# Performance work log

Hardware: AMD Instinct MI355X
Metric: run time of the kernel (lower is better)

Reference implementation:

```python
import jax, jax.numpy as jnp
import numpy as np

D_MODEL = 2048
N_HEADS = 16
HEAD_DIM = D_MODEL // N_HEADS
ROPE_BASE = 10000.0


def rope(x):
    # x: [b, h, s, d]; matches the torch module exactly:
    # x1 = even dims, x2 = odd dims; output = concat([x1*cos - x2*sin, x1*sin + x2*cos], -1)
    b, h, s, d = x.shape
    theta = 1.0 / ROPE_BASE ** (jnp.arange(0, d, 2, dtype=jnp.float32) / d)  # [d/2]
    angles = jnp.arange(s, dtype=jnp.float32)[:, None] * theta[None, :]       # [s, d/2]
    cos = jnp.cos(angles)[None, None]  # [1,1,s,d/2]
    sin = jnp.sin(angles)[None, None]
    x1, x2 = x[..., ::2], x[..., 1::2]
    return jnp.concatenate([x1 * cos - x2 * sin, x1 * sin + x2 * cos], axis=-1)


def setup_inputs() -> dict:
    key = jax.random.key(0)
    ks = jax.random.split(key, 5)
    b, s = 2, 2048
    x = jax.random.normal(ks[0], (b, s, D_MODEL), dtype=jnp.float32)
    scale_in = 1.0 / np.sqrt(D_MODEL)
    Wqkv = jax.random.normal(ks[1], (D_MODEL, 3 * D_MODEL), dtype=jnp.float32) * scale_in
    bqkv = jnp.zeros((3 * D_MODEL,), dtype=jnp.float32)
    Wo = jax.random.normal(ks[2], (D_MODEL, D_MODEL), dtype=jnp.float32) * scale_in
    bo = jnp.zeros((D_MODEL,), dtype=jnp.float32)
    return {"x": x, "Wqkv": Wqkv, "bqkv": bqkv, "Wo": Wo, "bo": bo}


def reference(x, Wqkv, bqkv, Wo, bo):
    b, s, d = x.shape
    qkv = x @ Wqkv + bqkv                      # [b, s, 3d]
    q, k, v = jnp.split(qkv, 3, axis=-1)
    def to_heads(t):
        return t.reshape(b, s, N_HEADS, HEAD_DIM).transpose(0, 2, 1, 3)  # [b,h,s,hd]
    q, k, v = to_heads(q), to_heads(k), to_heads(v)
    q = rope(q)
    k = rope(k)
    scores = jnp.einsum('bhqd,bhkd->bhqk', q, k) / jnp.sqrt(jnp.float32(HEAD_DIM))
    attn = jax.nn.softmax(scores, axis=-1)
    out = jnp.einsum('bhqk,bhkd->bhqd', attn, v)
    out = out.transpose(0, 2, 1, 3).reshape(b, s, d)
    return out @ Wo + bo
```

## Files before the change

kernel.cpp:

```cpp
#include <hip/hip_runtime.h>
#include <hip/hip_bf16.h>
#include <cstdint>
#include <type_traits>

#define D_MODEL 2048
#define NH 16
#define HD 128
#define SEQ 2048
#define QKV_LD (3 * D_MODEL)

typedef __attribute__((ext_vector_type(8))) short short8;
typedef __attribute__((ext_vector_type(4))) float f32x4;
typedef __attribute__((ext_vector_type(16))) float f32x16;

__device__ __forceinline__ ushort f2bf(float f) {
    union { float f; uint32_t u; } c; c.f = f;
    uint32_t u = c.u;
    uint32_t r = (u + 0x7FFFu + ((u >> 16) & 1u)) >> 16;
    return (ushort)r;
}
__device__ __forceinline__ float bf2f(ushort b) {
    union { uint32_t u; float f; } c; c.u = ((uint32_t)b) << 16;
    return c.f;
}

__global__ void cvt_bf16_kernel(const float* __restrict__ in, ushort* __restrict__ out, int n4) {
    int idx = blockIdx.x * blockDim.x + threadIdx.x;
    if (idx >= n4) return;
    float4 v = ((const float4*)in)[idx];
    ushort4 o;
    o.x = f2bf(v.x); o.y = f2bf(v.y); o.z = f2bf(v.z); o.w = f2bf(v.w);
    ((ushort4*)out)[idx] = o;
}

__global__ void transpose_bf16_kernel(const float* __restrict__ in, ushort* __restrict__ out,
                                      int R, int C) {
    __shared__ float tile[32][33];
    int tx = threadIdx.x, ty = threadIdx.y;
    int c0 = blockIdx.x * 32, r0 = blockIdx.y * 32;
    for (int i = 0; i < 4; ++i) {
        int r = r0 + ty + i * 8;
        tile[ty + i * 8][tx] = in[(size_t)r * C + c0 + tx];
    }
    __syncthreads();
    for (int i = 0; i < 4; ++i) {
        int c = c0 + ty + i * 8;
        out[(size_t)c * R + r0 + tx] = f2bf(tile[tx][ty + i * 8]);
    }
}

template <typename OutT>
__global__ __launch_bounds__(256) void gemm_bt_bias(
    const ushort* __restrict__ A,
    const ushort* __restrict__ Bt,
    const float* __restrict__ bias,
    OutT* __restrict__ C,
    int M, int N, int K)
{
    __shared__ ushort As[128 * 32];
    __shared__ ushort Bs[128 * 32];
    int t = threadIdx.x;
    int m0 = blockIdx.y * 128, n0 = blockIdx.x * 128;
    int wave = t >> 6, lane = t & 63;
    int wm = (wave & 1) * 64, wn = (wave >> 1) * 64;
    int lr = lane & 15, lh = lane >> 4;

    f32x4 acc[4][4];
    for (int i = 0; i < 4; i++)
        for (int j = 0; j < 4; j++)
            acc[i][j] = (f32x4)0.0f;

    int srow = t >> 2;
    int scol = (t & 3) * 8;
    const ushort* Ag = A + (size_t)(m0 + srow) * K + scol;
    const ushort* Bg = Bt + (size_t)(n0 + srow) * K + scol;

    for (int k0 = 0; k0 < K; k0 += 32) {
        __syncthreads();
        {
            uint4 a0 = *(const uint4*)(Ag + k0);
            uint4 a1 = *(const uint4*)(Ag + (size_t)64 * K + k0);
            uint4 b0 = *(const uint4*)(Bg + k0);
            uint4 b1 = *(const uint4*)(Bg + (size_t)64 * K + k0);
            *(uint4*)(As + srow * 32 + scol) = a0;
            *(uint4*)(As + (srow + 64) * 32 + scol) = a1;
            *(uint4*)(Bs + srow * 32 + scol) = b0;
            *(uint4*)(Bs + (srow + 64) * 32 + scol) = b1;
        }
        __syncthreads();
        short8 a[4], b[4];
        for (int i = 0; i < 4; i++)
            a[i] = *(const short8*)(As + (wm + i * 16 + lr) * 32 + lh * 8);
        for (int j = 0; j < 4; j++)
            b[j] = *(const short8*)(Bs + (wn + j * 16 + lr) * 32 + lh * 8);
        for (int i = 0; i < 4; i++)
            for (int j = 0; j < 4; j++)
                acc[i][j] = __builtin_amdgcn_mfma_f32_16x16x32_bf16(a[i], b[j], acc[i][j], 0, 0, 0);
    }

    for (int i = 0; i < 4; i++) {
        int row = m0 + wm + i * 16 + lh * 4;
        for (int j = 0; j < 4; j++) {
            int col = n0 + wn + j * 16 + lr;
            float bv = bias[col];
            for (int r = 0; r < 4; r++) {
                float v = acc[i][j][r] + bv;
                if constexpr (std::is_same<OutT, ushort>::value)
                    C[(size_t)(row + r) * N + col] = f2bf(v);
                else
                    C[(size_t)(row + r) * N + col] = v;
            }
        }
    }
}

__global__ void rope_cast_qk(const ushort* __restrict__ qkv,
                             ushort* __restrict__ Qb, ushort* __restrict__ Kb) {
    int t = threadIdx.x;
    int wv = blockIdx.x * 4 + (t >> 6);
    int j = t & 63;
    int bs = wv >> 5;
    int rem = wv & 31;
    int which = rem >> 4;
    int h = rem & 15;
    int s = bs & 2047;
    int b = bs >> 11;
    size_t src = (size_t)bs * QKV_LD + which * D_MODEL + h * HD;
    uint32_t pr = *(const uint32_t*)(qkv + src + 2 * j);
    float x1 = bf2f((ushort)(pr & 0xffff));
    float x2 = bf2f((ushort)(pr >> 16));
    float theta = powf(10000.0f, -(float)j * (1.0f / 64.0f));
    float ang = (float)s * theta;
    float sn, cs;
    sincosf(ang, &sn, &cs);
    float sc = which ? 1.0f : 0.08838834764831845f;
    float o1 = (x1 * cs - x2 * sn) * sc;
    float o2 = (x1 * sn + x2 * cs) * sc;
    ushort* dst = which ? Kb : Qb;
    size_t obase = ((size_t)(b * NH + h) * SEQ + s) * HD;
    dst[obase + j] = f2bf(o1);
    dst[obase + 64 + j] = f2bf(o2);
}

__global__ void v_transpose(const ushort* __restrict__ qkv, ushort* __restrict__ Vt) {
    __shared__ ushort tile[32][33];
    int tx = threadIdx.x, ty = threadIdx.y;
    int s0 = blockIdx.x * 32;
    int d0 = blockIdx.y * 32;
    int bh = blockIdx.z;
    int b = bh >> 4, h = bh & 15;
    for (int i = 0; i < 4; ++i) {
        int s = s0 + ty + i * 8;
        tile[ty + i * 8][tx] = qkv[((size_t)(b * SEQ + s)) * QKV_LD + 2 * D_MODEL + h * HD + d0 + tx];
    }
    __syncthreads();
    for (int i = 0; i < 4; ++i) {
        int d = d0 + ty + i * 8;
        Vt[((size_t)bh * HD + d) * SEQ + s0 + tx] = tile[tx][ty + i * 8];
    }
}

__global__ __launch_bounds__(256) void attn_mfma(const ushort* __restrict__ Qb,
                                                 const ushort* __restrict__ Kb,
                                                 const ushort* __restrict__ Vt,
                                                 ushort* __restrict__ ctx) {
    __shared__ ushort smem[25600];
    ushort* Ks = smem;
    ushort* Vts = smem + 8192;
    ushort* Ps = smem + 16384;

    int t = threadIdx.x;
    int w = t >> 6, l = t & 63;
    int l31 = l & 31, g = l >> 5;
    int q0 = blockIdx.x * 128;
    int bh = blockIdx.y;
    int b = bh >> 4, h = bh & 15;

    int qrow = q0 + w * 32 + l31;
    const ushort* Qg = Qb + ((size_t)bh * SEQ + qrow) * HD;
    short8 qf[8];
#pragma unroll
    for (int kc = 0; kc < 8; kc++)
        qf[kc] = *(const short8*)(Qg + kc * 16 + g * 8);

    f32x16 O[4];
#pragma unroll
    for (int di = 0; di < 4; di++) O[di] = (f32x16)0.0f;
    float m_run = -INFINITY, l_run = 0.0f;

    const ushort* KgB = Kb + (size_t)bh * SEQ * HD;
    const ushort* VtB = Vt + (size_t)bh * HD * SEQ;

    for (int k0 = 0; k0 < SEQ; k0 += 64) {
        __syncthreads();
#pragma unroll
        for (int c2 = 0; c2 < 4; c2++) {
            int f = c2 * 256 + t;
            int r = f >> 4, c = f & 15;
            int cp = c ^ (r & 15);
            uint4 v = *(const uint4*)(KgB + (size_t)(k0 + r) * HD + c * 8);
            *(uint4*)(Ks + r * 128 + cp * 8) = v;
        }
#pragma unroll
        for (int c2 = 0; c2 < 4; c2++) {
            int f = c2 * 256 + t;
            int d = f >> 3, c = f & 7;
            int cp = c ^ (d & 7);
            uint4 v = *(const uint4*)(VtB + (size_t)d * SEQ + k0 + c * 8);
            *(uint4*)(Vts + d * 64 + cp * 8) = v;
        }
        __syncthreads();

        f32x16 St[2];
        St[0] = (f32x16)0.0f;
        St[1] = (f32x16)0.0f;
#pragma unroll
        for (int ki = 0; ki < 2; ki++) {
            int row = ki * 32 + l31;
#pragma unroll
            for (int kc = 0; kc < 8; kc++) {
                int cp = (kc * 2 + g) ^ (row & 15);
                short8 a = *(const short8*)(Ks + row * 128 + cp * 8);
                St[ki] = __builtin_amdgcn_mfma_f32_32x32x16_bf16(a, qf[kc], St[ki], 0, 0, 0);
            }
        }

        float mx = -INFINITY;
#pragma unroll
        for (int ki = 0; ki < 2; ki++)
#pragma unroll
            for (int r = 0; r < 16; r++) mx = fmaxf(mx, St[ki][r]);
        mx = fmaxf(mx, __shfl_xor(mx, 32));
        float mn = fmaxf(m_run, mx);
        float alpha = __expf(m_run - mn);
        m_run = mn;
        float psum = 0.0f;
#pragma unroll
        for (int ki = 0; ki < 2; ki++)
#pragma unroll
            for (int r = 0; r < 16; r++) {
                float p = __expf(St[ki][r] - mn);
                St[ki][r] = p;
                psum += p;
            }
        psum += __shfl_xor(psum, 32);
        l_run = l_run * alpha + psum;
#pragma unroll
        for (int di = 0; di < 4; di++)
#pragma unroll
            for (int r = 0; r < 16; r++) O[di][r] *= alpha;

        {
            int qloc = w * 32 + l31;
            ushort* Pr = Ps + qloc * 72;
#pragma unroll
            for (int ki = 0; ki < 2; ki++)
#pragma unroll
                for (int u = 0; u < 4; u++) {
                    ushort4 pk;
                    pk.x = f2bf(St[ki][4 * u + 0]);
                    pk.y = f2bf(St[ki][4 * u + 1]);
                    pk.z = f2bf(St[ki][4 * u + 2]);
                    pk.w = f2bf(St[ki][4 * u + 3]);
                    *(ushort4*)(Pr + ki * 32 + 8 * u + 4 * g) = pk;
                }
        }

        {
            int qloc = w * 32 + l31;
            short8 pb[4];
#pragma unroll
            for (int kc = 0; kc < 4; kc++)
                pb[kc] = *(const short8*)(Ps + qloc * 72 + kc * 16 + g * 8);
#pragma unroll
            for (int di = 0; di < 4; di++) {
                int d = di * 32 + l31;
#pragma unroll
                for (int kc = 0; kc < 4; kc++) {
                    int cp = (kc * 2 + g) ^ (d & 7);
                    short8 va = *(const short8*)(Vts + d * 64 + cp * 8);
                    O[di] = __builtin_amdgcn_mfma_f32_32x32x16_bf16(va, pb[kc], O[di], 0, 0, 0);
                }
            }
        }
    }

    __syncthreads();
    float inv = 1.0f / l_run;
    ushort* ob = smem;
    {
        int qloc = w * 32 + l31;
        ushort* orow = ob + qloc * 128;
#pragma unroll
        for (int di = 0; di < 4; di++)
#pragma unroll
            for (int u = 0; u < 4; u++) {
                ushort4 pk;
                pk.x = f2bf(O[di][4 * u + 0] * inv);
                pk.y = f2bf(O[di][4 * u + 1] * inv);
                pk.z = f2bf(O[di][4 * u + 2] * inv);
                pk.w = f2bf(O[di][4 * u + 3] * inv);
                *(ushort4*)(orow + di * 32 + 8 * u + 4 * g) = pk;
            }
    }
#pragma unroll
    for (int p = 0; p < 8; p++) {
        int qloc = w * 32 + p * 4 + (l >> 4);
        int c16 = l & 15;
        uint4 v = *(const uint4*)(ob + qloc * 128 + c16 * 8);
        size_t tok = (size_t)b * SEQ + q0 + qloc;
        *(uint4*)(ctx + tok * D_MODEL + h * HD + c16 * 8) = v;
    }
}

extern "C" void kernel_launch(void* const* d_in, const int* in_sizes, int n_in,
                              void* d_out, int out_size, void* d_ws, size_t ws_size,
                              hipStream_t stream) {
    const float* x    = (const float*)d_in[0];
    const float* Wqkv = (const float*)d_in[1];
    const float* bqkv = (const float*)d_in[2];
    const float* Wo   = (const float*)d_in[3];
    const float* bo   = (const float*)d_in[4];
    float* out = (float*)d_out;

    char* ws = (char*)d_ws;
    ushort* x_bf   = (ushort*)(ws);
    ushort* wqkvT  = (ushort*)(ws + 16777216);
    ushort* woT    = (ushort*)(ws + 41943040);
    ushort* qkv_bf = (ushort*)(ws + 50331648);
    ushort* Qb     = (ushort*)(ws + 100663296);
    ushort* Kb     = (ushort*)(ws + 117440512);
    ushort* VtG    = (ushort*)(ws + 134217728);
    ushort* ctx    = (ushort*)(ws + 150994944);

    cvt_bf16_kernel<<<8192, 256, 0, stream>>>(x, x_bf, 2097152);
    transpose_bf16_kernel<<<dim3(192, 64), dim3(32, 8), 0, stream>>>(Wqkv, wqkvT, 2048, 6144);
    transpose_bf16_kernel<<<dim3(64, 64), dim3(32, 8), 0, stream>>>(Wo, woT, 2048, 2048);
    gemm_bt_bias<ushort><<<dim3(48, 32), 256, 0, stream>>>(x_bf, wqkvT, bqkv, qkv_bf, 4096, 6144, 2048);
    rope_cast_qk<<<32768, 256, 0, stream>>>(qkv_bf, Qb, Kb);
    v_transpose<<<dim3(64, 4, 32), dim3(32, 8), 0, stream>>>(qkv_bf, VtG);
    attn_mfma<<<dim3(16, 32), 256, 0, stream>>>(Qb, Kb, VtG, ctx);
    gemm_bt_bias<float><<<dim3(16, 32), 256, 0, stream>>>(ctx, woT, bo, out, 4096, 2048, 2048);
}
```

Before: 481.6 us.

## Load GEMM and attention tiles directly into LDS, with double-buffered prefetch of K

Replaces register-staged global-to-LDS copies with global_load_lds 16-byte direct loads in both the GEMM and the attention kernels. The RoPE and V-transpose kernels now write K and Vt already in the XOR-swizzled order the attention kernel reads, so tiles can be copied linearly. K tiles are double-buffered and the next tile is prefetched while the current one is used. V is loaded early and made visible by a new barrier before the PV stage. The aim is to cut VGPR staging and to overlap load latency with MFMA work. The cost is more LDS per block and an extra barrier per iteration.

```diff
diff --git a/kernel.cpp b/kernel.cpp
--- a/kernel.cpp
+++ b/kernel.cpp
@@ -22,6 +22,13 @@
 __device__ __forceinline__ float bf2f(ushort b) {
     union { uint32_t u; float f; } c; c.u = ((uint32_t)b) << 16;
     return c.f;
+}
+
+__device__ __forceinline__ void gl_lds16(const ushort* g, ushort* l) {
+    __builtin_amdgcn_global_load_lds(
+        (const __attribute__((address_space(1))) uint32_t*)g,
+        (__attribute__((address_space(3))) uint32_t*)l,
+        16, 0, 0);
 }
 
 __global__ void cvt_bf16_kernel(const float* __restrict__ in, ushort* __restrict__ out, int n4) {
@@ -57,8 +64,8 @@
     OutT* __restrict__ C,
     int M, int N, int K)
 {
-    __shared__ ushort As[128 * 32];
-    __shared__ ushort Bs[128 * 32];
+    __shared__ __align__(16) ushort As[128 * 32];
+    __shared__ __align__(16) ushort Bs[128 * 32];
     int t = threadIdx.x;
     int m0 = blockIdx.y * 128, n0 = blockIdx.x * 128;
     int wave = t >> 6, lane = t & 63;
@@ -70,23 +77,17 @@
         for (int j = 0; j < 4; j++)
             acc[i][j] = (f32x4)0.0f;
 
-    int srow = t >> 2;
-    int scol = (t & 3) * 8;
-    const ushort* Ag = A + (size_t)(m0 + srow) * K + scol;
-    const ushort* Bg = Bt + (size_t)(n0 + srow) * K + scol;
+    const ushort* Ag = A + (size_t)(m0 + (t >> 2)) * K + (t & 3) * 8;
+    const ushort* Bg = Bt + (size_t)(n0 + (t >> 2)) * K + (t & 3) * 8;
+    ushort* Asl = As + t * 8;
+    ushort* Bsl = Bs + t * 8;
 
     for (int k0 = 0; k0 < K; k0 += 32) {
         __syncthreads();
-        {
-            uint4 a0 = *(const uint4*)(Ag + k0);
-            uint4 a1 = *(const uint4*)(Ag + (size_t)64 * K + k0);
-            uint4 b0 = *(const uint4*)(Bg + k0);
-            uint4 b1 = *(const uint4*)(Bg + (size_t)64 * K + k0);
-            *(uint4*)(As + srow * 32 + scol) = a0;
-            *(uint4*)(As + (srow + 64) * 32 + scol) = a1;
-            *(uint4*)(Bs + srow * 32 + scol) = b0;
-            *(uint4*)(Bs + (srow + 64) * 32 + scol) = b1;
-        }
+        gl_lds16(Ag + k0, Asl);
+        gl_lds16(Ag + (size_t)64 * K + k0, Asl + 2048);
+        gl_lds16(Bg + k0, Bsl);
+        gl_lds16(Bg + (size_t)64 * K + k0, Bsl + 2048);
         __syncthreads();
         short8 a[4], b[4];
         for (int i = 0; i < 4; i++)
@@ -136,10 +137,17 @@
     float sc = which ? 1.0f : 0.08838834764831845f;
     float o1 = (x1 * cs - x2 * sn) * sc;
     float o2 = (x1 * sn + x2 * cs) * sc;
-    ushort* dst = which ? Kb : Qb;
     size_t obase = ((size_t)(b * NH + h) * SEQ + s) * HD;
-    dst[obase + j] = f2bf(o1);
-    dst[obase + 64 + j] = f2bf(o2);
+    int d1 = j, d2 = 64 + j;
+    if (which) {
+        int p1 = ((((d1 >> 3) ^ (s & 15)) << 3) | (d1 & 7));
+        int p2 = ((((d2 >> 3) ^ (s & 15)) << 3) | (d2 & 7));
+        Kb[obase + p1] = f2bf(o1);
+        Kb[obase + p2] = f2bf(o2);
+    } else {
+        Qb[obase + d1] = f2bf(o1);
+        Qb[obase + d2] = f2bf(o2);
+    }
 }
 
 __global__ void v_transpose(const ushort* __restrict__ qkv, ushort* __restrict__ Vt) {
@@ -154,9 +162,11 @@
         tile[ty + i * 8][tx] = qkv[((size_t)(b * SEQ + s)) * QKV_LD + 2 * D_MODEL + h * HD + d0 + tx];
     }
     __syncthreads();
+    int s = s0 + tx;
     for (int i = 0; i < 4; ++i) {
         int d = d0 + ty + i * 8;
-        Vt[((size_t)bh * HD + d) * SEQ + s0 + tx] = tile[tx][ty + i * 8];
+        int pos = (s & ~63) | (((((s >> 3) & 7) ^ (d & 7)) << 3)) | (s & 7);
+        Vt[((size_t)bh * HD + d) * SEQ + pos] = tile[tx][ty + i * 8];
     }
 }
 
@@ -164,10 +174,9 @@
                                                  const ushort* __restrict__ Kb,
                                                  const ushort* __restrict__ Vt,
                                                  ushort* __restrict__ ctx) {
-    __shared__ ushort smem[25600];
-    ushort* Ks = smem;
-    ushort* Vts = smem + 8192;
-    ushort* Ps = smem + 16384;
+    __shared__ __align__(16) ushort smem[33792];
+    ushort* Vts = smem + 16384;
+    ushort* Ps  = smem + 24576;
 
     int t = threadIdx.x;
     int w = t >> 6, l = t & 63;
@@ -176,6 +185,9 @@
     int bh = blockIdx.y;
     int b = bh >> 4, h = bh & 15;
 
+    const ushort* KgB = Kb + (size_t)bh * SEQ * HD;
+    const ushort* VtB = Vt + (size_t)bh * HD * SEQ;
+
     int qrow = q0 + w * 32 + l31;
     const ushort* Qg = Qb + ((size_t)bh * SEQ + qrow) * HD;
     short8 qf[8];
@@ -188,28 +200,30 @@
     for (int di = 0; di < 4; di++) O[di] = (f32x16)0.0f;
     float m_run = -INFINITY, l_run = 0.0f;
 
-    const ushort* KgB = Kb + (size_t)bh * SEQ * HD;
-    const ushort* VtB = Vt + (size_t)bh * HD * SEQ;
-
-    for (int k0 = 0; k0 < SEQ; k0 += 64) {
+#pragma unroll
+    for (int c2 = 0; c2 < 4; c2++) {
+        int f = c2 * 256 + t;
+        gl_lds16(KgB + (size_t)(f >> 4) * HD + (f & 15) * 8, smem + f * 8);
+    }
+
+    for (int it = 0; it < SEQ / 64; it++) {
+        int k0 = it * 64;
+        ushort* Kcur = smem + (it & 1) * 8192;
+        ushort* Knxt = smem + ((it + 1) & 1) * 8192;
         __syncthreads();
+
 #pragma unroll
         for (int c2 = 0; c2 < 4; c2++) {
             int f = c2 * 256 + t;
-            int r = f >> 4, c = f & 15;
-            int cp = c ^ (r & 15);
-            uint4 v = *(const uint4*)(KgB + (size_t)(k0 + r) * HD + c * 8);
-            *(uint4*)(Ks + r * 128 + cp * 8) = v;
-        }
-#pragma unroll
-        for (int c2 = 0; c2 < 4; c2++) {
-            int f = c2 * 256 + t;
-            int d = f >> 3, c = f & 7;
-            int cp = c ^ (d & 7);
-            uint4 v = *(const uint4*)(VtB + (size_t)d * SEQ + k0 + c * 8);
-            *(uint4*)(Vts + d * 64 + cp * 8) = v;
-        }
-        __syncthreads();
+            gl_lds16(VtB + (size_t)(f >> 3) * SEQ + k0 + (f & 7) * 8, Vts + f * 8);
+        }
+        if (it + 1 < SEQ / 64) {
+#pragma unroll
+            for (int c2 = 0; c2 < 4; c2++) {
+                int f = c2 * 256 + t;
+                gl_lds16(KgB + (size_t)(k0 + 64 + (f >> 4)) * HD + (f & 15) * 8, Knxt + f * 8);
+            }
+        }
 
         f32x16 St[2];
         St[0] = (f32x16)0.0f;
@@ -220,7 +234,7 @@
 #pragma unroll
             for (int kc = 0; kc < 8; kc++) {
                 int cp = (kc * 2 + g) ^ (row & 15);
-                short8 a = *(const short8*)(Ks + row * 128 + cp * 8);
+                short8 a = *(const short8*)(Kcur + row * 128 + cp * 8);
                 St[ki] = __builtin_amdgcn_mfma_f32_32x32x16_bf16(a, qf[kc], St[ki], 0, 0, 0);
             }
         }
@@ -265,6 +279,8 @@
                     *(ushort4*)(Pr + ki * 32 + 8 * u + 4 * g) = pk;
                 }
         }
+
+        __syncthreads();
 
         {
             int qloc = w * 32 + l31;
```

After: 535.5 us. 11.2% more time.

## Prefetch next K/V and GEMM tiles into registers to overlap loads with MFMA

Applied to the files above, without the earlier changes.

Both the GEMM and the attention kernel now issue the global loads for the next k-tile into registers right after the shared-memory barrier, then store them to LDS at the top of the following iteration. This is register double-buffering, meant to hide global-memory latency behind the MFMA work of the current tile. The attention kernel also precomputes its swizzled load and store offsets once and gains a launch_bounds minimum of 2 blocks. The extra live registers (32 VGPRs for K/V in attention) may raise register pressure or force spills under the new occupancy hint.

```diff
diff --git a/kernel.cpp b/kernel.cpp
--- a/kernel.cpp
+++ b/kernel.cpp
@@ -57,8 +57,8 @@
     OutT* __restrict__ C,
     int M, int N, int K)
 {
-    __shared__ ushort As[128 * 32];
-    __shared__ ushort Bs[128 * 32];
+    __shared__ __align__(16) ushort As[128 * 32];
+    __shared__ __align__(16) ushort Bs[128 * 32];
     int t = threadIdx.x;
     int m0 = blockIdx.y * 128, n0 = blockIdx.x * 128;
     int wave = t >> 6, lane = t & 63;
@@ -75,19 +75,24 @@
     const ushort* Ag = A + (size_t)(m0 + srow) * K + scol;
     const ushort* Bg = Bt + (size_t)(n0 + srow) * K + scol;
 
+    uint4 ar0 = *(const uint4*)(Ag);
+    uint4 ar1 = *(const uint4*)(Ag + (size_t)64 * K);
+    uint4 br0 = *(const uint4*)(Bg);
+    uint4 br1 = *(const uint4*)(Bg + (size_t)64 * K);
+
     for (int k0 = 0; k0 < K; k0 += 32) {
         __syncthreads();
-        {
-            uint4 a0 = *(const uint4*)(Ag + k0);
-            uint4 a1 = *(const uint4*)(Ag + (size_t)64 * K + k0);
-            uint4 b0 = *(const uint4*)(Bg + k0);
-            uint4 b1 = *(const uint4*)(Bg + (size_t)64 * K + k0);
-            *(uint4*)(As + srow * 32 + scol) = a0;
-            *(uint4*)(As + (srow + 64) * 32 + scol) = a1;
-            *(uint4*)(Bs + srow * 32 + scol) = b0;
-            *(uint4*)(Bs + (srow + 64) * 32 + scol) = b1;
-        }
+        *(uint4*)(As + srow * 32 + scol) = ar0;
+        *(uint4*)(As + (srow + 64) * 32 + scol) = ar1;
+        *(uint4*)(Bs + srow * 32 + scol) = br0;
+        *(uint4*)(Bs + (srow + 64) * 32 + scol) = br1;
         __syncthreads();
+        if (k0 + 32 < K) {
+            ar0 = *(const uint4*)(Ag + k0 + 32);
+            ar1 = *(const uint4*)(Ag + (size_t)64 * K + k0 + 32);
+            br0 = *(const uint4*)(Bg + k0 + 32);
+            br1 = *(const uint4*)(Bg + (size_t)64 * K + k0 + 32);
+        }
         short8 a[4], b[4];
         for (int i = 0; i < 4; i++)
             a[i] = *(const short8*)(As + (wm + i * 16 + lr) * 32 + lh * 8);
@@ -160,14 +165,14 @@
     }
 }
 
-__global__ __launch_bounds__(256) void attn_mfma(const ushort* __restrict__ Qb,
-                                                 const ushort* __restrict__ Kb,
-                                                 const ushort* __restrict__ Vt,
-                                                 ushort* __restrict__ ctx) {
-    __shared__ ushort smem[25600];
-    ushort* Ks = smem;
+__global__ __launch_bounds__(256, 2) void attn_mfma(const ushort* __restrict__ Qb,
+                                                    const ushort* __restrict__ Kb,
+                                                    const ushort* __restrict__ Vt,
+                                                    ushort* __restrict__ ctx) {
+    __shared__ __align__(16) ushort smem[25600];
+    ushort* Ks  = smem;
     ushort* Vts = smem + 8192;
-    ushort* Ps = smem + 16384;
+    ushort* Ps  = smem + 16384;
 
     int t = threadIdx.x;
     int w = t >> 6, l = t & 63;
@@ -176,6 +181,9 @@
     int bh = blockIdx.y;
     int b = bh >> 4, h = bh & 15;
 
+    const ushort* KgB = Kb + (size_t)bh * SEQ * HD;
+    const ushort* VtB = Vt + (size_t)bh * HD * SEQ;
+
     int qrow = q0 + w * 32 + l31;
     const ushort* Qg = Qb + ((size_t)bh * SEQ + qrow) * HD;
     short8 qf[8];
@@ -188,28 +196,40 @@
     for (int di = 0; di < 4; di++) O[di] = (f32x16)0.0f;
     float m_run = -INFINITY, l_run = 0.0f;
 
-    const ushort* KgB = Kb + (size_t)bh * SEQ * HD;
-    const ushort* VtB = Vt + (size_t)bh * HD * SEQ;
-
-    for (int k0 = 0; k0 < SEQ; k0 += 64) {
+    int offKg[4], offKl[4], offVg[4], offVl[4];
+#pragma unroll
+    for (int c2 = 0; c2 < 4; c2++) {
+        int f = c2 * 256 + t;
+        int r = f >> 4, c = f & 15;
+        offKg[c2] = r * HD + c * 8;
+        offKl[c2] = r * 128 + (c ^ (r & 15)) * 8;
+        int d = f >> 3, cv = f & 7;
+        offVg[c2] = d * SEQ + cv * 8;
+        offVl[c2] = d * 64 + (cv ^ (d & 7)) * 8;
+    }
+    uint4 kreg[4], vreg[4];
+#pragma unroll
+    for (int c2 = 0; c2 < 4; c2++) {
+        kreg[c2] = *(const uint4*)(KgB + offKg[c2]);
+        vreg[c2] = *(const uint4*)(VtB + offVg[c2]);
+    }
+
+    for (int it = 0; it < SEQ / 64; it++) {
+        int k0 = it * 64;
         __syncthreads();
 #pragma unroll
         for (int c2 = 0; c2 < 4; c2++) {
-            int f = c2 * 256 + t;
-            int r = f >> 4, c = f & 15;
-            int cp = c ^ (r & 15);
-            uint4 v = *(const uint4*)(KgB + (size_t)(k0 + r) * HD + c * 8);
-            *(uint4*)(Ks + r * 128 + cp * 8) = v;
-        }
-#pragma unroll
-        for (int c2 = 0; c2 < 4; c2++) {
-            int f = c2 * 256 + t;
-            int d = f >> 3, c = f & 7;
-            int cp = c ^ (d & 7);
-            uint4 v = *(const uint4*)(VtB + (size_t)d * SEQ + k0 + c * 8);
-            *(uint4*)(Vts + d * 64 + cp * 8) = v;
+            *(uint4*)(Ks + offKl[c2]) = kreg[c2];
+            *(uint4*)(Vts + offVl[c2]) = vreg[c2];
         }
         __syncthreads();
+        if (it + 1 < SEQ / 64) {
+#pragma unroll
+            for (int c2 = 0; c2 < 4; c2++) {
+                kreg[c2] = *(const uint4*)(KgB + (size_t)(k0 + 64) * HD + offKg[c2]);
+                vreg[c2] = *(const uint4*)(VtB + (k0 + 64) + offVg[c2]);
+            }
+        }
 
         f32x16 St[2];
         St[0] = (f32x16)0.0f;
```

Result: slower. 577.6 us (+19.9%).
